# Kernel tuning notes

Measured on AMD Instinct MI355X. Metric: run time of the kernel, lower is better.

## Reference

```python
import jax, jax.numpy as jnp
import numpy as np
import math

B, T, F, H, A = 32, 2048, 2048, 1024, 512


def setup_inputs() -> dict:
    key = jax.random.key(0)
    ks = jax.random.split(key, 8)
    def xavier(k, shape):
        fan_out, fan_in = shape
        bound = math.sqrt(6.0 / (fan_in + fan_out))
        return jax.random.uniform(k, shape, jnp.float32, -bound, bound)
    return {
        "features": jax.random.normal(ks[0], (B, T, F), jnp.float32),
        "hidden": jax.random.normal(ks[1], (B, H), jnp.float32),
        "W_h": xavier(ks[2], (A, H)),
        "b_h": jnp.zeros((A,), jnp.float32),
        "W_a": xavier(ks[3], (A, F)),
        "b_a": jnp.zeros((A,), jnp.float32),
        "v_w": xavier(ks[4], (1, A)),
        "v_b": jnp.zeros((1,), jnp.float32),
    }


def reference(features, hidden, W_h, b_h, W_a, b_a, v_w, v_b):
    # h_proj: [B, 1, A]; a_proj: [B, T, A]
    h_proj = (hidden @ W_h.T + b_h)[:, None, :]
    a_proj = jnp.einsum('btf,af->bta', features, W_a) + b_a
    # energy: [B, T]
    energy = (jnp.tanh(h_proj + a_proj) @ v_w[0] + v_b[0]) / math.sqrt(W_h.shape[0])
    alpha = jax.nn.softmax(energy, axis=1)
    context = jnp.einsum('bt,btf->bf', alpha, features)
    return (context, alpha)
```

## Files before the change

kernel.cpp:

```cpp
#include <hip/hip_runtime.h>
#include <hip/hip_bf16.h>
#include <math.h>

#define B_ 32
#define T_ 2048
#define F_ 2048
#define H_ 1024
#define A_ 512

typedef __attribute__((ext_vector_type(8))) short short8;
typedef __attribute__((ext_vector_type(4))) float f32x4;

__device__ __forceinline__ unsigned short f2bf(float x) {
  union { float f; unsigned int u; } v; v.f = x;
  unsigned int r = v.u + 0x7FFFu + ((v.u >> 16) & 1u);
  return (unsigned short)(r >> 16);
}

#define GLOAD_LDS16(gp, lp) __builtin_amdgcn_global_load_lds( \
    (const __attribute__((address_space(1))) void*)(gp), \
    (__attribute__((address_space(3))) void*)(lp), 16, 0, 0)

#define SBAR   asm volatile("s_barrier" ::: "memory")
#define SCHEDB __builtin_amdgcn_sched_barrier(0)

__global__ __launch_bounds__(256) void k_convert_wa(const float* __restrict__ wa,
                                                    unsigned short* __restrict__ out) {
  int i = (blockIdx.x * 256 + threadIdx.x) * 4;
  float4 v = *(const float4*)(wa + i);
  ushort4 o;
  o.x = f2bf(v.x); o.y = f2bf(v.y); o.z = f2bf(v.z); o.w = f2bf(v.w);
  *(ushort4*)(out + i) = o;
}

__global__ __launch_bounds__(256) void k_hproj(const float* __restrict__ hidden,
                                               const float* __restrict__ Wh,
                                               const float* __restrict__ bh,
                                               const float* __restrict__ ba,
                                               float* __restrict__ hcomb) {
  int gw = (blockIdx.x * 256 + threadIdx.x) >> 6;
  int lane = threadIdx.x & 63;
  int b = gw >> 9, a = gw & 511;
  const float* wr = Wh + a * H_;
  const float* hr = hidden + b * H_;
  float acc = 0.f;
  #pragma unroll
  for (int k = 0; k < H_; k += 256) {
    float4 wv = *(const float4*)(wr + k + lane * 4);
    float4 hv = *(const float4*)(hr + k + lane * 4);
    acc += wv.x * hv.x + wv.y * hv.y + wv.z * hv.z + wv.w * hv.w;
  }
  #pragma unroll
  for (int off = 32; off; off >>= 1) acc += __shfl_xor(acc, off);
  if (lane == 0) hcomb[gw] = acc + bh[a] + ba[a];
}

__global__ __launch_bounds__(512, 4) void k_energy(
    const float* __restrict__ feat, const unsigned short* __restrict__ wab,
    const float* __restrict__ hcomb, const float* __restrict__ vw,
    const float* __restrict__ vb, float* __restrict__ energy) {
  __shared__ __align__(16) char smem[81920];

  const int tid = threadIdx.x;
  const int lane = tid & 63;
  const int w = tid >> 6;
  const int wm = w >> 2, wn = w & 3;
  const int lrow = lane & 15;
  const int m0 = blockIdx.x * 64;
  const int bb = m0 >> 11;

  const int brow = tid >> 3;
  const unsigned short* const bsrc0 = wab + (size_t)brow * 2048 +
      (((((tid & 7) << 4) ^ ((brow & 7) << 4)) >> 1));
  char* const ldsb = smem + w * 1024;

  const int arow = tid >> 3;
  const float* const asrc = feat + (size_t)(m0 + arow) * F_ + ((tid & 7) << 3);
  const int aw_byte = (arow << 7) + ((((tid & 7) << 4)) ^ ((arow & 7) << 4));

  const int xbase = ((lane >> 4) << 4) ^ ((lane & 7) << 4);
  const int a_row_byte = (wm * 32 + lrow) << 7;
  const int b_row_byte = (wn * 128 + lrow) << 7;

  f32x4 acc[2][8] = {};

  {
    float4 av0 = *(const float4*)(asrc);
    float4 av1 = *(const float4*)(asrc + 4);
    #pragma unroll
    for (int r = 0; r < 8; ++r)
      GLOAD_LDS16(bsrc0 + r * (64 * 2048), ldsb + r * 8192);
    short8 apk;
    apk[0] = (short)f2bf(av0.x); apk[1] = (short)f2bf(av0.y);
    apk[2] = (short)f2bf(av0.z); apk[3] = (short)f2bf(av0.w);
    apk[4] = (short)f2bf(av1.x); apk[5] = (short)f2bf(av1.y);
    apk[6] = (short)f2bf(av1.z); apk[7] = (short)f2bf(av1.w);
    *(short8*)(smem + 65536 + aw_byte) = apk;
    __syncthreads();
  }

#define COMPUTE_TILE(CURBUF) do {                                             \
    const char* As_ = smem + 65536 + (CURBUF) * 8192;                         \
    _Pragma("unroll")                                                         \
    for (int kk = 0; kk < 2; ++kk) {                                          \
      const int xo = xbase ^ (kk << 6);                                       \
      const char* Ab = As_ + a_row_byte + xo;                                 \
      const char* Bb = smem + b_row_byte + xo;                                \
      short8 a0 = *(const short8*)(Ab);                                       \
      short8 a1 = *(const short8*)(Ab + 2048);                                \
      short8 b0 = *(const short8*)(Bb);                                       \
      short8 b1 = *(const short8*)(Bb + 2048);                                \
      short8 b2 = *(const short8*)(Bb + 4096);                                \
      short8 b3 = *(const short8*)(Bb + 6144);                                \
      acc[0][0] = __builtin_amdgcn_mfma_f32_16x16x32_bf16(a0, b0, acc[0][0], 0, 0, 0); \
      acc[1][0] = __builtin_amdgcn_mfma_f32_16x16x32_bf16(a1, b0, acc[1][0], 0, 0, 0); \
      acc[0][1] = __builtin_amdgcn_mfma_f32_16x16x32_bf16(a0, b1, acc[0][1], 0, 0, 0); \
      acc[1][1] = __builtin_amdgcn_mfma_f32_16x16x32_bf16(a1, b1, acc[1][1], 0, 0, 0); \
      acc[0][2] = __builtin_amdgcn_mfma_f32_16x16x32_bf16(a0, b2, acc[0][2], 0, 0, 0); \
      acc[1][2] = __builtin_amdgcn_mfma_f32_16x16x32_bf16(a1, b2, acc[1][2], 0, 0, 0); \
      acc[0][3] = __builtin_amdgcn_mfma_f32_16x16x32_bf16(a0, b3, acc[0][3], 0, 0, 0); \
      acc[1][3] = __builtin_amdgcn_mfma_f32_16x16x32_bf16(a1, b3, acc[1][3], 0, 0, 0); \
      short8 b4 = *(const short8*)(Bb + 8192);                                \
      short8 b5 = *(const short8*)(Bb + 10240);                               \
      short8 b6 = *(const short8*)(Bb + 12288);                               \
      short8 b7 = *(const short8*)(Bb + 14336);                               \
      acc[0][4] = __builtin_amdgcn_mfma_f32_16x16x32_bf16(a0, b4, acc[0][4], 0, 0, 0); \
      acc[1][4] = __builtin_amdgcn_mfma_f32_16x16x32_bf16(a1, b4, acc[1][4], 0, 0, 0); \
      acc[0][5] = __builtin_amdgcn_mfma_f32_16x16x32_bf16(a0, b5, acc[0][5], 0, 0, 0); \
      acc[1][5] = __builtin_amdgcn_mfma_f32_16x16x32_bf16(a1, b5, acc[1][5], 0, 0, 0); \
      acc[0][6] = __builtin_amdgcn_mfma_f32_16x16x32_bf16(a0, b6, acc[0][6], 0, 0, 0); \
      acc[1][6] = __builtin_amdgcn_mfma_f32_16x16x32_bf16(a1, b6, acc[1][6], 0, 0, 0); \
      acc[0][7] = __builtin_amdgcn_mfma_f32_16x16x32_bf16(a0, b7, acc[0][7], 0, 0, 0); \
      acc[1][7] = __builtin_amdgcn_mfma_f32_16x16x32_bf16(a1, b7, acc[1][7], 0, 0, 0); \
    }                                                                         \
  } while (0)

  #pragma unroll 1
  for (int t = 0; t < 31; ++t) {
    const int cur = t & 1, nxt = cur ^ 1;
    const int k1 = (t + 1) << 6;
    float4 av0 = *(const float4*)(asrc + k1);
    float4 av1 = *(const float4*)(asrc + k1 + 4);
    SCHEDB;
    COMPUTE_TILE(cur);
    SBAR;
    const unsigned short* bs = bsrc0 + k1;
    #pragma unroll
    for (int r = 0; r < 8; ++r)
      GLOAD_LDS16(bs + r * (64 * 2048), ldsb + r * 8192);
    short8 apk;
    apk[0] = (short)f2bf(av0.x); apk[1] = (short)f2bf(av0.y);
    apk[2] = (short)f2bf(av0.z); apk[3] = (short)f2bf(av0.w);
    apk[4] = (short)f2bf(av1.x); apk[5] = (short)f2bf(av1.y);
    apk[6] = (short)f2bf(av1.z); apk[7] = (short)f2bf(av1.w);
    *(short8*)(smem + 65536 + nxt * 8192 + aw_byte) = apk;
    __syncthreads();
  }
  COMPUTE_TILE(1);
#undef COMPUTE_TILE

  float hv[8], vv[8];
  #pragma unroll
  for (int ni = 0; ni < 8; ++ni) {
    int col = wn * 128 + ni * 16 + lrow;
    hv[ni] = hcomb[bb * 512 + col];
    vv[ni] = vw[col];
  }
  float (*e_red)[4] = (float(*)[4])(smem + 65536);
  __syncthreads();
  const float vbv = vb[0];
  #pragma unroll
  for (int mi = 0; mi < 2; ++mi) {
    #pragma unroll
    for (int j = 0; j < 4; ++j) {
      float s = 0.f;
      #pragma unroll
      for (int ni = 0; ni < 8; ++ni) {
        float x = acc[mi][ni][j] + hv[ni];
        s += tanhf(x) * vv[ni];
      }
      s += __shfl_xor(s, 1); s += __shfl_xor(s, 2);
      s += __shfl_xor(s, 4); s += __shfl_xor(s, 8);
      if (lrow == 0) e_red[wm * 32 + mi * 16 + (lane >> 4) * 4 + j][wn] = s;
    }
  }
  __syncthreads();
  if (tid < 64) {
    float s = e_red[tid][0] + e_red[tid][1] + e_red[tid][2] + e_red[tid][3];
    energy[m0 + tid] = (s + vbv) * 0.04419417382415922f;
  }
}

__global__ __launch_bounds__(256) void k_softmax(const float* __restrict__ energy,
                                                 float* __restrict__ alpha) {
  const int b = blockIdx.x, tid = threadIdx.x;
  const float* e = energy + b * T_;
  float4 v0 = ((const float4*)e)[tid * 2];
  float4 v1 = ((const float4*)e)[tid * 2 + 1];
  float m = fmaxf(fmaxf(fmaxf(v0.x, v0.y), fmaxf(v0.z, v0.w)),
                  fmaxf(fmaxf(v1.x, v1.y), fmaxf(v1.z, v1.w)));
  #pragma unroll
  for (int off = 32; off; off >>= 1) m = fmaxf(m, __shfl_xor(m, off));
  __shared__ float rmax[4], rsum[4];
  const int lane = tid & 63, wv = tid >> 6;
  if (!lane) rmax[wv] = m;
  __syncthreads();
  m = fmaxf(fmaxf(rmax[0], rmax[1]), fmaxf(rmax[2], rmax[3]));
  float x0 = expf(v0.x - m), x1 = expf(v0.y - m), x2 = expf(v0.z - m), x3 = expf(v0.w - m);
  float x4 = expf(v1.x - m), x5 = expf(v1.y - m), x6 = expf(v1.z - m), x7 = expf(v1.w - m);
  float s = ((x0 + x1) + (x2 + x3)) + ((x4 + x5) + (x6 + x7));
  #pragma unroll
  for (int off = 32; off; off >>= 1) s += __shfl_xor(s, off);
  if (!lane) rsum[wv] = s;
  __syncthreads();
  s = (rsum[0] + rsum[1]) + (rsum[2] + rsum[3]);
  float inv = 1.f / s;
  float4 o0 = {x0 * inv, x1 * inv, x2 * inv, x3 * inv};
  float4 o1 = {x4 * inv, x5 * inv, x6 * inv, x7 * inv};
  float* ao = alpha + b * T_;
  ((float4*)ao)[tid * 2] = o0;
  ((float4*)ao)[tid * 2 + 1] = o1;
}

__global__ __launch_bounds__(256) void k_ctx_partial(const float* __restrict__ feat,
                                                     const float* __restrict__ alpha,
                                                     float* __restrict__ part) {
  const int b = blockIdx.x, fh = blockIdx.y, tc = blockIdx.z;
  const int tid = threadIdx.x;
  __shared__ float sa[128];
  if (tid < 128) sa[tid] = alpha[b * T_ + tc * 128 + tid];
  __syncthreads();
  const int f = fh * 1024 + tid * 4;
  const float* fp = feat + ((size_t)(b * T_ + tc * 128)) * F_ + f;
  float4 s = {0.f, 0.f, 0.f, 0.f};
  #pragma unroll 4
  for (int t = 0; t < 128; ++t) {
    float a = sa[t];
    float4 v = *(const float4*)(fp + (size_t)t * F_);
    s.x += a * v.x; s.y += a * v.y; s.z += a * v.z; s.w += a * v.w;
  }
  *(float4*)(part + ((size_t)(b * 16 + tc)) * F_ + f) = s;
}

__global__ __launch_bounds__(256) void k_ctx_reduce(const float* __restrict__ part,
                                                    float* __restrict__ ctx) {
  const int i4 = blockIdx.x * 256 + threadIdx.x;
  const int b = i4 >> 9, f4 = i4 & 511;
  const float4* p = (const float4*)part;
  float4 s = {0.f, 0.f, 0.f, 0.f};
  #pragma unroll
  for (int tc = 0; tc < 16; ++tc) {
    float4 v = p[((b * 16 + tc) << 9) + f4];
    s.x += v.x; s.y += v.y; s.z += v.z; s.w += v.w;
  }
  ((float4*)ctx)[i4] = s;
}

extern "C" void kernel_launch(void* const* d_in, const int* in_sizes, int n_in,
                              void* d_out, int out_size, void* d_ws, size_t ws_size,
                              hipStream_t stream) {
  const float* feat   = (const float*)d_in[0];
  const float* hidden = (const float*)d_in[1];
  const float* Wh     = (const float*)d_in[2];
  const float* bh     = (const float*)d_in[3];
  const float* Wa     = (const float*)d_in[4];
  const float* ba     = (const float*)d_in[5];
  const float* vw     = (const float*)d_in[6];
  const float* vb     = (const float*)d_in[7];

  float* ctx   = (float*)d_out;
  float* alpha = (float*)d_out + B_ * T_;

  char* ws = (char*)d_ws;
  unsigned short* wab = (unsigned short*)ws;
  float* hcomb  = (float*)(ws + 2097152);
  float* energy = (float*)(ws + 2097152 + 65536);
  float* part   = (float*)(ws + 2097152 + 65536 + 262144);

  k_convert_wa<<<dim3(1024), dim3(256), 0, stream>>>(Wa, wab);
  k_hproj<<<dim3(4096), dim3(256), 0, stream>>>(hidden, Wh, bh, ba, hcomb);
  k_energy<<<dim3(1024), dim3(512), 0, stream>>>(feat, wab, hcomb, vw, vb, energy);
  k_softmax<<<dim3(32), dim3(256), 0, stream>>>(energy, alpha);
  k_ctx_partial<<<dim3(32, 2, 16), dim3(256), 0, stream>>>(feat, alpha, part);
  k_ctx_reduce<<<dim3(64), dim3(256), 0, stream>>>(part, ctx);
}
```

Baseline: 299.9 us.

## Double-buffer W_a tile in LDS and prefetch features two tiles ahead

Makes the B-operand (bf16 W_a) LDS tile double-buffered so the async global-to-LDS load for the next K-step is issued before computing the current tile, removing the mid-iteration barrier. Feature rows are now prefetched two steps ahead in registers, and an explicit vmcnt/lgkmcnt wait replaces __syncthreads. LDS use grows to 144KB and launch bounds drop to 2 blocks per CU, trading occupancy for deeper overlap of loads and MFMA work.

```diff
diff --git a/kernel.cpp b/kernel.cpp
--- a/kernel.cpp
+++ b/kernel.cpp
@@ -23,6 +23,7 @@
 
 #define SBAR   asm volatile("s_barrier" ::: "memory")
 #define SCHEDB __builtin_amdgcn_sched_barrier(0)
+#define WAIT_V2_L0 asm volatile("s_waitcnt vmcnt(2) lgkmcnt(0)" ::: "memory")
 
 __global__ __launch_bounds__(256) void k_convert_wa(const float* __restrict__ wa,
                                                     unsigned short* __restrict__ out) {
@@ -55,11 +56,11 @@
   if (lane == 0) hcomb[gw] = acc + bh[a] + ba[a];
 }
 
-__global__ __launch_bounds__(512, 4) void k_energy(
+__global__ __launch_bounds__(512, 2) void k_energy(
     const float* __restrict__ feat, const unsigned short* __restrict__ wab,
     const float* __restrict__ hcomb, const float* __restrict__ vw,
     const float* __restrict__ vb, float* __restrict__ energy) {
-  __shared__ __align__(16) char smem[81920];
+  __shared__ __align__(16) char smem[147456];
 
   const int tid = threadIdx.x;
   const int lane = tid & 63;
@@ -72,7 +73,6 @@
   const int brow = tid >> 3;
   const unsigned short* const bsrc0 = wab + (size_t)brow * 2048 +
       (((((tid & 7) << 4) ^ ((brow & 7) << 4)) >> 1));
-  char* const ldsb = smem + w * 1024;
 
   const int arow = tid >> 3;
   const float* const asrc = feat + (size_t)(m0 + arow) * F_ + ((tid & 7) << 3);
@@ -83,29 +83,33 @@
   const int b_row_byte = (wn * 128 + lrow) << 7;
 
   f32x4 acc[2][8] = {};
-
-  {
-    float4 av0 = *(const float4*)(asrc);
-    float4 av1 = *(const float4*)(asrc + 4);
-    #pragma unroll
-    for (int r = 0; r < 8; ++r)
-      GLOAD_LDS16(bsrc0 + r * (64 * 2048), ldsb + r * 8192);
-    short8 apk;
-    apk[0] = (short)f2bf(av0.x); apk[1] = (short)f2bf(av0.y);
-    apk[2] = (short)f2bf(av0.z); apk[3] = (short)f2bf(av0.w);
-    apk[4] = (short)f2bf(av1.x); apk[5] = (short)f2bf(av1.y);
-    apk[6] = (short)f2bf(av1.z); apk[7] = (short)f2bf(av1.w);
-    *(short8*)(smem + 65536 + aw_byte) = apk;
-    __syncthreads();
-  }
+  float4 avA0, avA1, avB0, avB1;
+
+#define STAGE_B(NXT, KB) do {                                                 \
+    const unsigned short* bs_ = bsrc0 + (KB);                                 \
+    char* bd_ = smem + (NXT) * 65536 + w * 1024;                              \
+    _Pragma("unroll")                                                         \
+    for (int r_ = 0; r_ < 8; ++r_)                                            \
+      GLOAD_LDS16(bs_ + r_ * (64 * 2048), bd_ + r_ * 8192);                   \
+  } while (0)
+
+#define CVT_A(NXT, V0, V1) do {                                               \
+    short8 apk_;                                                              \
+    apk_[0] = (short)f2bf((V0).x); apk_[1] = (short)f2bf((V0).y);             \
+    apk_[2] = (short)f2bf((V0).z); apk_[3] = (short)f2bf((V0).w);             \
+    apk_[4] = (short)f2bf((V1).x); apk_[5] = (short)f2bf((V1).y);             \
+    apk_[6] = (short)f2bf((V1).z); apk_[7] = (short)f2bf((V1).w);             \
+    *(short8*)(smem + 131072 + (NXT) * 8192 + aw_byte) = apk_;                \
+  } while (0)
 
 #define COMPUTE_TILE(CURBUF) do {                                             \
-    const char* As_ = smem + 65536 + (CURBUF) * 8192;                         \
+    const char* As_ = smem + 131072 + (CURBUF) * 8192;                        \
+    const char* Bs_ = smem + (CURBUF) * 65536;                                \
     _Pragma("unroll")                                                         \
     for (int kk = 0; kk < 2; ++kk) {                                          \
       const int xo = xbase ^ (kk << 6);                                       \
       const char* Ab = As_ + a_row_byte + xo;                                 \
-      const char* Bb = smem + b_row_byte + xo;                                \
+      const char* Bb = Bs_ + b_row_byte + xo;                                 \
       short8 a0 = *(const short8*)(Ab);                                       \
       short8 a1 = *(const short8*)(Ab + 2048);                                \
       short8 b0 = *(const short8*)(Bb);                                       \
@@ -135,29 +139,45 @@
     }                                                                         \
   } while (0)
 
+  {
+    avA0 = *(const float4*)(asrc);
+    avA1 = *(const float4*)(asrc + 4);
+    STAGE_B(0, 0);
+    SCHEDB;
+    avB0 = *(const float4*)(asrc + 64);
+    avB1 = *(const float4*)(asrc + 68);
+    SCHEDB;
+    CVT_A(0, avA0, avA1);
+    SCHEDB;
+    WAIT_V2_L0;
+    SBAR;
+  }
+
+#define ITER(CUR, NXT, LD0, LD1, CV0, CV1, T) do {                            \
+    STAGE_B(NXT, ((T) + 1) << 6);                                             \
+    SCHEDB;                                                                   \
+    LD0 = *(const float4*)(asrc + ((((T) + 2) & 31) << 6));                   \
+    LD1 = *(const float4*)(asrc + ((((T) + 2) & 31) << 6) + 4);               \
+    SCHEDB;                                                                   \
+    COMPUTE_TILE(CUR);                                                        \
+    CVT_A(NXT, CV0, CV1);                                                     \
+    SCHEDB;                                                                   \
+    WAIT_V2_L0;                                                               \
+    SBAR;                                                                     \
+  } while (0)
+
   #pragma unroll 1
-  for (int t = 0; t < 31; ++t) {
-    const int cur = t & 1, nxt = cur ^ 1;
-    const int k1 = (t + 1) << 6;
-    float4 av0 = *(const float4*)(asrc + k1);
-    float4 av1 = *(const float4*)(asrc + k1 + 4);
-    SCHEDB;
-    COMPUTE_TILE(cur);
-    SBAR;
-    const unsigned short* bs = bsrc0 + k1;
-    #pragma unroll
-    for (int r = 0; r < 8; ++r)
-      GLOAD_LDS16(bs + r * (64 * 2048), ldsb + r * 8192);
-    short8 apk;
-    apk[0] = (short)f2bf(av0.x); apk[1] = (short)f2bf(av0.y);
-    apk[2] = (short)f2bf(av0.z); apk[3] = (short)f2bf(av0.w);
-    apk[4] = (short)f2bf(av1.x); apk[5] = (short)f2bf(av1.y);
-    apk[6] = (short)f2bf(av1.z); apk[7] = (short)f2bf(av1.w);
-    *(short8*)(smem + 65536 + nxt * 8192 + aw_byte) = apk;
-    __syncthreads();
-  }
+  for (int tt = 0; tt < 15; ++tt) {
+    const int t = tt * 2;
+    ITER(0, 1, avA0, avA1, avB0, avB1, t);
+    ITER(1, 0, avB0, avB1, avA0, avA1, t + 1);
+  }
+  ITER(0, 1, avA0, avA1, avB0, avB1, 30);
   COMPUTE_TILE(1);
+#undef ITER
 #undef COMPUTE_TILE
+#undef CVT_A
+#undef STAGE_B
 
   float hv[8], vv[8];
   #pragma unroll
@@ -166,7 +186,7 @@
     hv[ni] = hcomb[bb * 512 + col];
     vv[ni] = vw[col];
   }
-  float (*e_red)[4] = (float(*)[4])(smem + 65536);
+  float (*e_red)[4] = (float(*)[4])(smem);
   __syncthreads();
   const float vbv = vb[0];
   #pragma unroll
```

New measurement: 331.6 us. 1.11x slower.
